# Optimization experiments

Hardware: AMD Instinct MI355X
Metric: run time of the kernel (lower is better)

## Reference

```python
import jax, jax.numpy as jnp
import numpy as np

# Quantization constants from the original module
X_ZP = -66   # int8 zero point
Y_ZP = 160   # uint8 zero point


def setup_inputs() -> dict:
    key = jax.random.key(0)
    k1, k2 = jax.random.split(key)
    # x: [7, B, M, K] int8 in [-128, 127]
    x = jax.random.randint(k1, (7, 8, 512, 1024), -128, 128, dtype=jnp.int32).astype(jnp.int8)
    # y: [B, K, N] uint8 in [0, 255]
    y = jax.random.randint(k2, (8, 1024, 512), 0, 256, dtype=jnp.int32).astype(jnp.uint8)
    return {
        "x": x,
        "y": y,
        "x_scale": jnp.float32(0.03),
        "y_scale": jnp.float32(0.025),
    }


def reference(x, y, x_scale, y_scale):
    # dequantize_per_tensor: (q - zero_point) * scale
    xf = (x.astype(jnp.float32) - jnp.float32(X_ZP)) * x_scale   # [7, B, M, K]
    yf = (y.astype(jnp.float32) - jnp.float32(Y_ZP)) * y_scale   # [B, K, N]
    # torch.matmul broadcast: [7,B,M,K] @ [B,K,N] -> [7,B,M,N]
    return jnp.einsum('gbmk,bkn->gbmn', xf, yf)
```

## Files before the change

### kernel.cpp

```cpp
#include <hip/hip_runtime.h>
#include <stdint.h>

#define AS1 __attribute__((address_space(1)))
#define AS3 __attribute__((address_space(3)))

typedef int v4i __attribute__((ext_vector_type(4)));

constexpr int G = 7, B = 8, M = 512, N = 512, K = 1024;
constexpr int GBn = G * B;

constexpr size_t X8_BYTES = (size_t)GBn * M * K;
constexpr size_t YT_BYTES = (size_t)B * N * K;
constexpr size_t RS_CNT   = (size_t)GBn * M;
constexpr size_t CS_CNT   = (size_t)B * N;
constexpr size_t WS_NEEDED = X8_BYTES + YT_BYTES + RS_CNT * 4 + CS_CNT * 4;

__global__ __launch_bounds__(256) void transpose_pack_y(const int* __restrict__ y,
                                                        signed char* __restrict__ yt) {
    __shared__ unsigned char tile[64][80];
    int n0 = blockIdx.x * 64;
    int k0 = blockIdx.y * 64;
    int b  = blockIdx.z;
    int t  = threadIdx.x;

    int r  = t >> 2;
    int c0 = (t & 3) * 16;
    const int* src = y + ((size_t)b * K + k0 + r) * N + n0 + c0;
    uint32_t p[4];
#pragma unroll
    for (int q = 0; q < 4; ++q) {
        int4 v = ((const int4*)src)[q];
        p[q] =  (uint32_t)((v.x & 255) ^ 128)
             | ((uint32_t)((v.y & 255) ^ 128) << 8)
             | ((uint32_t)((v.z & 255) ^ 128) << 16)
             | ((uint32_t)((v.w & 255) ^ 128) << 24);
    }
    *(uint4*)&tile[r][c0] = make_uint4(p[0], p[1], p[2], p[3]);
    __syncthreads();

    int nl = t >> 2;
    int kc = (t & 3) * 16;
    uint32_t q[4];
#pragma unroll
    for (int w = 0; w < 4; ++w) {
        uint32_t b0 = tile[kc + w * 4 + 0][nl];
        uint32_t b1 = tile[kc + w * 4 + 1][nl];
        uint32_t b2 = tile[kc + w * 4 + 2][nl];
        uint32_t b3 = tile[kc + w * 4 + 3][nl];
        q[w] = b0 | (b1 << 8) | (b2 << 16) | (b3 << 24);
    }
    *(uint4*)(yt + ((size_t)b * N + n0 + nl) * K + k0 + kc) = make_uint4(q[0], q[1], q[2], q[3]);
}

__device__ __forceinline__ int wave_reduce_sum(int v) {
#pragma unroll
    for (int off = 32; off > 0; off >>= 1) v += __shfl_down(v, off, 64);
    return v;
}

__global__ __launch_bounds__(256) void pack_x_sums(const int* __restrict__ x,
                                                   signed char* __restrict__ x8,
                                                   const signed char* __restrict__ yt,
                                                   int* __restrict__ rowsum,
                                                   int* __restrict__ colsum) {
    int wave = threadIdx.x >> 6, lane = threadIdx.x & 63;
    int row = blockIdx.x * 4 + wave;
    if (row < (int)(GBn * M)) {
        const int* src = x + (size_t)row * K + lane * 16;
        int s = 0;
        uint32_t p[4];
#pragma unroll
        for (int q = 0; q < 4; ++q) {
            int4 v = ((const int4*)src)[q];
            s += v.x + v.y + v.z + v.w;
            p[q] =  (uint32_t)(v.x & 255)
                 | ((uint32_t)(v.y & 255) << 8)
                 | ((uint32_t)(v.z & 255) << 16)
                 | ((uint32_t)(v.w & 255) << 24);
        }
        *(uint4*)(x8 + (size_t)row * K + lane * 16) = make_uint4(p[0], p[1], p[2], p[3]);
        s = wave_reduce_sum(s);
        if (lane == 0) rowsum[row] = s;
    } else {
        int rr = row - (int)(GBn * M);
        uint4 u = *(const uint4*)(yt + (size_t)rr * K + lane * 16);
        uint32_t wds[4] = {u.x, u.y, u.z, u.w};
        int s = 0;
#pragma unroll
        for (int q = 0; q < 4; ++q) {
            uint32_t w = wds[q];
            s += (int)(signed char)(w) + (int)(signed char)(w >> 8)
               + (int)(signed char)(w >> 16) + (int)(signed char)(w >> 24);
        }
        s = wave_reduce_sum(s);
        if (lane == 0) colsum[rr] = s;
    }
}

__global__ __launch_bounds__(256, 2) void gemm_i8(const signed char* __restrict__ x8,
                                                  const signed char* __restrict__ yt,
                                                  const int* __restrict__ rowsum,
                                                  const int* __restrict__ colsum,
                                                  const float* __restrict__ xsp,
                                                  const float* __restrict__ ysp,
                                                  float* __restrict__ out) {
    __shared__ signed char As[128 * 64];
    __shared__ signed char Bs[128 * 64];

    int tile = blockIdx.x;
    int gb   = blockIdx.y;
    int mt = tile >> 2, nt = tile & 3;
    int b  = gb & 7;
    int tid = threadIdx.x, wave = tid >> 6, lane = tid & 63;
    int wm = (wave >> 1) * 64, wn = (wave & 1) * 64;

    const signed char* Ab = x8 + ((size_t)(gb * M + mt * 128 + wave * 32 + (lane >> 2))) * K + (lane & 3) * 16;
    const signed char* Bb = yt + ((size_t)(b  * N + nt * 128 + wave * 32 + (lane >> 2))) * K + (lane & 3) * 16;
    signed char* AsW = As + wave * 2048;
    signed char* BsW = Bs + wave * 2048;

    v4i zero = {0, 0, 0, 0};
    v4i acc[4][4];
#pragma unroll
    for (int i = 0; i < 4; ++i)
#pragma unroll
        for (int j = 0; j < 4; ++j) acc[i][j] = zero;

    int fr = lane & 15;
    int fk = (lane >> 4) * 16;

    for (int k0 = 0; k0 < K; k0 += 64) {
#pragma unroll
        for (int c = 0; c < 2; ++c) {
            __builtin_amdgcn_global_load_lds((const AS1 uint32_t*)(Ab + (size_t)c * 16 * K + k0),
                                             (AS3 uint32_t*)(AsW + c * 1024), 16, 0, 0);
            __builtin_amdgcn_global_load_lds((const AS1 uint32_t*)(Bb + (size_t)c * 16 * K + k0),
                                             (AS3 uint32_t*)(BsW + c * 1024), 16, 0, 0);
        }
        __syncthreads();

        v4i af[4], bf[4];
#pragma unroll
        for (int i = 0; i < 4; ++i)
            af[i] = *(const v4i*)(As + (wm + i * 16 + fr) * 64 + fk);
#pragma unroll
        for (int j = 0; j < 4; ++j)
            bf[j] = *(const v4i*)(Bs + (wn + j * 16 + fr) * 64 + fk);

#pragma unroll
        for (int i = 0; i < 4; ++i)
#pragma unroll
            for (int j = 0; j < 4; ++j)
                acc[i][j] = __builtin_amdgcn_mfma_i32_16x16x64_i8(af[i], bf[j], acc[i][j], 0, 0, 0);
        __syncthreads();
    }

    float s = xsp[0] * ysp[0];
    int colL = lane & 15;
    int rowQ = (lane >> 4) * 4;
    float* outg = out + (size_t)gb * M * N;
    const int* rs = rowsum + gb * M;
    const int* cs = colsum + b * N;
#pragma unroll
    for (int i = 0; i < 4; ++i) {
#pragma unroll
        for (int r = 0; r < 4; ++r) {
            int row_g = mt * 128 + wm + i * 16 + rowQ + r;
            int rsv = rs[row_g];
#pragma unroll
            for (int j = 0; j < 4; ++j) {
                int col_g = nt * 128 + wn + j * 16 + colL;
                int t = acc[i][j][r] - 32 * rsv + 66 * cs[col_g] - 2162688;
                outg[(size_t)row_g * N + col_g] = s * (float)t;
            }
        }
    }
}

__global__ __launch_bounds__(256) void naive_kernel(const int* __restrict__ x,
                                                    const int* __restrict__ y,
                                                    const float* __restrict__ xsp,
                                                    const float* __restrict__ ysp,
                                                    float* __restrict__ out) {
    size_t idx = (size_t)blockIdx.x * 256 + threadIdx.x;
    int n  = (int)(idx & 511);
    int m  = (int)((idx >> 9) & 511);
    int gb = (int)(idx >> 18);
    int b  = gb & 7;
    const int* xr = x + ((size_t)gb * M + m) * K;
    const int* yc = y + (size_t)b * K * N + n;
    int dot = 0, sx = 0, sy = 0;
    for (int k = 0; k < K; ++k) {
        int a = xr[k];
        int c = yc[(size_t)k * N];
        dot += a * c; sx += a; sy += c;
    }
    float s = xsp[0] * ysp[0];
    out[idx] = s * (float)(dot - 160 * sx + 66 * sy - 10813440);
}

extern "C" void kernel_launch(void* const* d_in, const int* in_sizes, int n_in,
                              void* d_out, int out_size, void* d_ws, size_t ws_size,
                              hipStream_t stream) {
    const int*   x  = (const int*)d_in[0];
    const int*   y  = (const int*)d_in[1];
    const float* xs = (const float*)d_in[2];
    const float* ys = (const float*)d_in[3];
    float* out = (float*)d_out;

    if (ws_size < WS_NEEDED) {
        naive_kernel<<<(14680064 + 255) / 256, 256, 0, stream>>>(x, y, xs, ys, out);
        return;
    }

    char* ws = (char*)d_ws;
    signed char* x8 = (signed char*)ws;
    signed char* yt = (signed char*)(ws + X8_BYTES);
    int* rowsum = (int*)(ws + X8_BYTES + YT_BYTES);
    int* colsum = rowsum + RS_CNT;

    transpose_pack_y<<<dim3(N / 64, K / 64, B), 256, 0, stream>>>(y, yt);
    pack_x_sums<<<(GBn * M + CS_CNT) / 4, 256, 0, stream>>>(x, x8, yt, rowsum, colsum);
    gemm_i8<<<dim3(16, GBn), 256, 0, stream>>>(x8, yt, rowsum, colsum, xs, ys, out);
}
```

Baseline: 228.5 us.

## Double-buffer per-wave LDS tiles with swizzle and drop block barriers in int8 GEMM

Restructures the int8 GEMM main loop so each wave loads only its own 64x64 A and B sub-tiles into private, double-buffered LDS. Loads are issued two stages ahead and synchronised with vmcnt/lgkmcnt waits instead of block-wide __syncthreads. An XOR swizzle on the 16-byte chunk index is meant to cut LDS bank conflicts on fragment reads. In exchange LDS use rises to 64KB per block, which may limit occupancy, and each wave now loads overlapping A/B rows redundantly, which raises global/L2 traffic.

```diff
diff --git a/kernel.cpp b/kernel.cpp
--- a/kernel.cpp
+++ b/kernel.cpp
@@ -104,58 +104,69 @@
                                                   const float* __restrict__ xsp,
                                                   const float* __restrict__ ysp,
                                                   float* __restrict__ out) {
-    __shared__ signed char As[128 * 64];
-    __shared__ signed char Bs[128 * 64];
-
-    int tile = blockIdx.x;
-    int gb   = blockIdx.y;
-    int mt = tile >> 2, nt = tile & 3;
+    __shared__ signed char lds[4][2][8192];
+
+    int mt = blockIdx.x, nt = blockIdx.y, gb = blockIdx.z;
     int b  = gb & 7;
-    int tid = threadIdx.x, wave = tid >> 6, lane = tid & 63;
-    int wm = (wave >> 1) * 64, wn = (wave & 1) * 64;
-
-    const signed char* Ab = x8 + ((size_t)(gb * M + mt * 128 + wave * 32 + (lane >> 2))) * K + (lane & 3) * 16;
-    const signed char* Bb = yt + ((size_t)(b  * N + nt * 128 + wave * 32 + (lane >> 2))) * K + (lane & 3) * 16;
-    signed char* AsW = As + wave * 2048;
-    signed char* BsW = Bs + wave * 2048;
-
-    v4i zero = {0, 0, 0, 0};
+    int tid = threadIdx.x, w = tid >> 6, lane = tid & 63;
+    int wm = (w >> 1) * 64, wn = (w & 1) * 64;
+
+    int chunk = ((lane & 3) ^ ((lane >> 3) & 3)) * 16;
+    const signed char* Ab = x8 + ((size_t)(gb * M + mt * 128 + wm + (lane >> 2))) * K + chunk;
+    const signed char* Bb = yt + ((size_t)(b  * N + nt * 128 + wn + (lane >> 2))) * K + chunk;
+    signed char* L = &lds[w][0][0];
+
+    int fr = lane & 15, q = lane >> 4;
+    int fko = (q ^ ((fr >> 1) & 3)) * 16;
+
     v4i acc[4][4];
 #pragma unroll
     for (int i = 0; i < 4; ++i)
 #pragma unroll
-        for (int j = 0; j < 4; ++j) acc[i][j] = zero;
-
-    int fr = lane & 15;
-    int fk = (lane >> 4) * 16;
-
-    for (int k0 = 0; k0 < K; k0 += 64) {
-#pragma unroll
-        for (int c = 0; c < 2; ++c) {
-            __builtin_amdgcn_global_load_lds((const AS1 uint32_t*)(Ab + (size_t)c * 16 * K + k0),
-                                             (AS3 uint32_t*)(AsW + c * 1024), 16, 0, 0);
-            __builtin_amdgcn_global_load_lds((const AS1 uint32_t*)(Bb + (size_t)c * 16 * K + k0),
-                                             (AS3 uint32_t*)(BsW + c * 1024), 16, 0, 0);
-        }
-        __syncthreads();
+        for (int j = 0; j < 4; ++j) acc[i][j] = (v4i){0, 0, 0, 0};
+
+#define STAGE(SIDX, BUF)                                                                  \
+    do {                                                                                  \
+        _Pragma("unroll")                                                                 \
+        for (int c = 0; c < 4; ++c)                                                       \
+            __builtin_amdgcn_global_load_lds(                                             \
+                (const AS1 uint32_t*)(Ab + (size_t)c * 16 * K + (SIDX) * 64),             \
+                (AS3 uint32_t*)(L + (BUF) * 8192 + c * 1024), 16, 0, 0);                  \
+        _Pragma("unroll")                                                                 \
+        for (int c = 0; c < 4; ++c)                                                       \
+            __builtin_amdgcn_global_load_lds(                                             \
+                (const AS1 uint32_t*)(Bb + (size_t)c * 16 * K + (SIDX) * 64),             \
+                (AS3 uint32_t*)(L + (BUF) * 8192 + 4096 + c * 1024), 16, 0, 0);           \
+    } while (0)
+
+    STAGE(0, 0);
+    STAGE(1, 1);
+
+    for (int s = 0; s < 16; ++s) {
+        int buf = s & 1;
+        if (s < 15) asm volatile("s_waitcnt vmcnt(8)" ::: "memory");
+        else        asm volatile("s_waitcnt vmcnt(0)" ::: "memory");
 
         v4i af[4], bf[4];
 #pragma unroll
         for (int i = 0; i < 4; ++i)
-            af[i] = *(const v4i*)(As + (wm + i * 16 + fr) * 64 + fk);
+            af[i] = *(const v4i*)(L + buf * 8192 + (i * 16 + fr) * 64 + fko);
 #pragma unroll
         for (int j = 0; j < 4; ++j)
-            bf[j] = *(const v4i*)(Bs + (wn + j * 16 + fr) * 64 + fk);
+            bf[j] = *(const v4i*)(L + buf * 8192 + 4096 + (j * 16 + fr) * 64 + fko);
+        asm volatile("s_waitcnt lgkmcnt(0)" ::: "memory");
+
+        if (s < 14) STAGE(s + 2, buf);
 
 #pragma unroll
         for (int i = 0; i < 4; ++i)
 #pragma unroll
             for (int j = 0; j < 4; ++j)
                 acc[i][j] = __builtin_amdgcn_mfma_i32_16x16x64_i8(af[i], bf[j], acc[i][j], 0, 0, 0);
-        __syncthreads();
-    }
-
-    float s = xsp[0] * ysp[0];
+    }
+#undef STAGE
+
+    float sc = xsp[0] * ysp[0];
     int colL = lane & 15;
     int rowQ = (lane >> 4) * 4;
     float* outg = out + (size_t)gb * M * N;
@@ -171,7 +182,7 @@
             for (int j = 0; j < 4; ++j) {
                 int col_g = nt * 128 + wn + j * 16 + colL;
                 int t = acc[i][j][r] - 32 * rsv + 66 * cs[col_g] - 2162688;
-                outg[(size_t)row_g * N + col_g] = s * (float)t;
+                outg[(size_t)row_g * N + col_g] = sc * (float)t;
             }
         }
     }
@@ -221,5 +232,5 @@
 
     transpose_pack_y<<<dim3(N / 64, K / 64, B), 256, 0, stream>>>(y, yt);
     pack_x_sums<<<(GBn * M + CS_CNT) / 4, 256, 0, stream>>>(x, x8, yt, rowsum, colsum);
-    gemm_i8<<<dim3(16, GBn), 256, 0, stream>>>(x8, yt, rowsum, colsum, xs, ys, out);
-}
+    gemm_i8<<<dim3(M / 128, N / 128, GBn), 256, 0, stream>>>(x8, yt, rowsum, colsum, xs, ys, out);
+}
```

After: 231.3 us. Within noise of the previous version (+1.2%).
